# Optimization experiments

Measured on AMD Instinct MI355X. Metric: run time of the kernel, lower is better.

Reference implementation:

```python
import jax, jax.numpy as jnp
import numpy as np

HEAD_SIZE = 64


def setup_inputs() -> dict:
    key = jax.random.key(0)
    kx, kq, kk, kv = jax.random.split(key, 4)
    B, L, D = 4, 4096, 1024
    scale = 1.0 / np.sqrt(D)
    x = jax.random.normal(kx, (B, L, D), dtype=jnp.float32)
    Wq = jax.random.normal(kq, (D, HEAD_SIZE), dtype=jnp.float32) * scale
    Wk = jax.random.normal(kk, (D, HEAD_SIZE), dtype=jnp.float32) * scale
    Wv = jax.random.normal(kv, (D, HEAD_SIZE), dtype=jnp.float32) * scale
    return {"x": x, "Wq": Wq, "Wk": Wk, "Wv": Wv}


def reference(x, Wq, Wk, Wv):
    B, L, D = x.shape
    H = Wq.shape[1]
    q = jnp.einsum('bld,dh->blh', x, Wq)  # [B,L,H]
    k = jnp.einsum('bld,dh->blh', x, Wk)
    v = jnp.einsum('bld,dh->blh', x, Wv)
    # full L x L score matrix, as in the original module
    scores = jnp.einsum('bqh,bkh->bqk', q, k) / jnp.sqrt(jnp.float32(H))
    causal = jnp.tril(jnp.ones((L, L), dtype=bool))
    scores = jnp.where(causal, scores, -jnp.inf)
    attn = jax.nn.softmax(scores, axis=-1)
    z = jnp.einsum('bqk,bkh->bqh', attn, v)  # [B,L,H]
    return z
```

## Files before the change

kernel.cpp:

```cpp
#include <hip/hip_runtime.h>
#include <stdint.h>

#define L_SEQ 4096
#define D_MODEL 1024
#define HEAD 64
#define KCH 256
#define MAXCH 16
#define NQT 32

typedef unsigned short u16;
typedef _Float16 f16;
typedef __attribute__((ext_vector_type(8))) f16 f16x8;
typedef __attribute__((ext_vector_type(2))) __fp16 fp16x2;
typedef __attribute__((ext_vector_type(4))) float f32x4;

static __device__ __forceinline__ u16 f16bits(float f) {
    union { f16 h; u16 u; } c; c.h = (f16)f; return c.u;
}
static __device__ __forceinline__ uint32_t pk16(float a, float b) {
    union { fp16x2 h; uint32_t u; } c;
    c.h = __builtin_amdgcn_cvt_pkrtz(a, b);
    return c.u;
}
static __device__ __forceinline__ f16x8 ld8h(const u16* p) { return *(const f16x8*)p; }

static __device__ __forceinline__ f32x4 mfma16h(f16x8 a, f16x8 b, f32x4 c) {
    return __builtin_amdgcn_mfma_f32_16x16x32_f16(a, b, c, 0, 0, 0);
}

static __device__ __forceinline__ void gload16(const u16* g, u16* l) {
    __builtin_amdgcn_global_load_lds(
        (const __attribute__((address_space(1))) void*)g,
        (__attribute__((address_space(3))) void*)l, 16, 0, 0);
}

static __device__ __forceinline__ int Sq(int qt) {
    return (qt & 1) ? ((qt + 1) * (qt + 1)) >> 2 : (qt * (qt + 2)) >> 2;
}

__global__ __launch_bounds__(256) void conv_w(
    const float* __restrict__ Wq, const float* __restrict__ Wk,
    const float* __restrict__ Wv, u16* __restrict__ Wt)
{
    __shared__ u16 tile[64][72];
    const float* W = (blockIdx.y == 0) ? Wq : (blockIdx.y == 1) ? Wk : Wv;
    const float sc = (blockIdx.y == 0) ? 0.18033688f : 1.0f;
    u16* dst = Wt + blockIdx.y * (HEAD * D_MODEL);
    const int k0 = blockIdx.x * 64, t = threadIdx.x;
    #pragma unroll
    for (int i = 0; i < 16; i++) {
        int idx = i * 256 + t;
        int kk = idx >> 6, h = idx & 63;
        tile[h][kk] = f16bits(W[(size_t)(k0 + kk) * HEAD + h] * sc);
    }
    __syncthreads();
    #pragma unroll
    for (int i = 0; i < 16; i++) {
        int idx = i * 256 + t;
        int h = idx >> 6, kk = idx & 63;
        dst[(size_t)h * D_MODEL + k0 + kk] = tile[h][kk];
    }
}

__global__ __launch_bounds__(256) void qkv_proj(
    const float* __restrict__ x, const u16* __restrict__ Wt,
    u16* __restrict__ qb, u16* __restrict__ kb, u16* __restrict__ vTb)
{
    __shared__ __align__(16) u16 Wl[2 * 2 * 192 * 32];
    __shared__ __align__(16) u16 Xl[2 * 2 * 32 * 36];
#define WLX(bb,dh,r,c) Wl[(((bb)*2 + (dh))*192 + (r))*32 + (c)]
#define XLX(bb,kh,r,c) Xl[(((bb)*2 + (kh))*32  + (r))*36 + (c)]
#define CT(r,c)        ((u16*)Wl)[(r)*200 + (c)]

    const int t = threadIdx.x;
    const int wv = t >> 6, lane = t & 63;
    const int ln16 = lane & 15, quad = lane >> 4;
    const int w3 = wv * 3;
    const int m0 = blockIdx.x * 32;

    f32x4 acc[2][3] = {};
    float4 xv0, xv1;

    auto issueW = [&](int s, int bb) {
        const int k0 = s * 64;
        #pragma unroll
        for (int k2 = 0; k2 < 6; k2++) {
            int c = wv * 6 + k2;
            int dh = c & 1, g = c >> 1;
            const u16* gp = Wt + (size_t)(g * 16 + (lane >> 2)) * D_MODEL
                               + k0 + dh * 32 + (lane & 3) * 8;
            gload16(gp, &WLX(bb, dh, g * 16 + (lane >> 2), (lane & 3) * 8));
        }
    };
    auto loadx = [&](int s) {
        const int k0 = s * 64;
        int r0 = t >> 4, cs0 = (t & 15) * 4;
        xv0 = *(const float4*)&x[(size_t)(m0 + r0) * D_MODEL + k0 + cs0];
        int idx = 256 + t, r1 = idx >> 4, cs1 = (idx & 15) * 4;
        xv1 = *(const float4*)&x[(size_t)(m0 + r1) * D_MODEL + k0 + cs1];
    };
    auto packx = [&](int bb) {
        int r0 = t >> 4, cs0 = (t & 15) * 4;
        uint2 p0; p0.x = pk16(xv0.x, xv0.y); p0.y = pk16(xv0.z, xv0.w);
        *(uint2*)&XLX(bb, cs0 >> 5, r0, cs0 & 31) = p0;
        int idx = 256 + t, r1 = idx >> 4, cs1 = (idx & 15) * 4;
        uint2 p1; p1.x = pk16(xv1.x, xv1.y); p1.y = pk16(xv1.z, xv1.w);
        *(uint2*)&XLX(bb, cs1 >> 5, r1, cs1 & 31) = p1;
    };

    loadx(0); issueW(0, 0); packx(0);
    int buf = 0;
    for (int s = 0; s < 16; s++) {
        __syncthreads();
        f16x8 xb[2][2], af[2][3];
        #pragma unroll
        for (int c = 0; c < 2; c++) {
            xb[c][0] = ld8h(&XLX(buf, c, ln16, quad * 8));
            xb[c][1] = ld8h(&XLX(buf, c, 16 + ln16, quad * 8));
            #pragma unroll
            for (int j = 0; j < 3; j++)
                af[c][j] = ld8h(&WLX(buf, c, (w3 + j) * 16 + ln16, quad * 8));
        }
        if (s + 1 < 16) { loadx(s + 1); issueW(s + 1, buf ^ 1); }
        #pragma unroll
        for (int c = 0; c < 2; c++)
            #pragma unroll
            for (int j = 0; j < 3; j++) {
                acc[0][j] = mfma16h(af[c][j], xb[c][0], acc[0][j]);
                acc[1][j] = mfma16h(af[c][j], xb[c][1], acc[1][j]);
            }
        if (s + 1 < 16) packx(buf ^ 1);
        buf ^= 1;
    }

    __syncthreads();
    #pragma unroll
    for (int mt = 0; mt < 2; mt++) {
        #pragma unroll
        for (int j = 0; j < 3; j++) {
            int g0 = (w3 + j) * 16 + quad * 4;
            uint2 pk;
            pk.x = pk16(acc[mt][j][0], acc[mt][j][1]);
            pk.y = pk16(acc[mt][j][2], acc[mt][j][3]);
            *(uint2*)&CT(mt * 16 + ln16, g0) = pk;
        }
    }
    __syncthreads();
    {
        int m = t >> 3, hg = (t & 7) * 8;
        *(f16x8*)&qb[(size_t)(m0 + m) * HEAD + hg] = *(f16x8*)&CT(m, hg);
        *(f16x8*)&kb[(size_t)(m0 + m) * HEAD + hg] = *(f16x8*)&CT(m, 64 + hg);
        int h = t >> 2, mg = (t & 3) * 8;
        f16x8 vvv;
        #pragma unroll
        for (int jj = 0; jj < 8; jj++)
            ((u16*)&vvv)[jj] = CT(mg + jj, 128 + h);
        int bbt = m0 >> 12, l0 = m0 & 4095;
        *(f16x8*)&vTb[(size_t)(bbt * HEAD + h) * L_SEQ + l0 + mg] = vvv;
    }
#undef WLX
#undef XLX
#undef CT
}

__global__ __launch_bounds__(256, 4) void attn_chunk(
    const u16* __restrict__ qb, const u16* __restrict__ kb,
    const u16* __restrict__ vT, float* __restrict__ Opart, float* __restrict__ lpart)
{
    const int qt = blockIdx.x, ch = blockIdx.y, b = blockIdx.z;
    if (ch * KCH > qt * 128 + 127) return;

    __shared__ __align__(16) u16 Kls[2 * 64 * 32];
    __shared__ __align__(16) u16 Vls[2 * 64 * 32];
    __shared__ __align__(16) u16 Pls[4 * 32 * 72];
#define KBX(dh,r,c) Kls[((dh)*64 + (r))*32 + (c)]
#define VBX(kh,r,c) Vls[((kh)*64 + (r))*32 + (c)]
#define PX(r,c)     Pls[((wv)*32 + (r))*72 + (c)]

    const int t = threadIdx.x, wv = t >> 6, lane = t & 63;
    const int ln16 = lane & 15, quad = lane >> 4;
    const int qmin = qt * 128 + wv * 32;

    f16x8 qf[2][2];
    #pragma unroll
    for (int qn = 0; qn < 2; qn++) {
        const u16* qrp = qb + (size_t)(b * L_SEQ + qmin + qn * 16 + ln16) * HEAD + quad * 8;
        qf[qn][0] = ld8h(qrp); qf[qn][1] = ld8h(qrp + 32);
    }

    const u16* kbb = kb + (size_t)b * L_SEQ * HEAD;
    const u16* vbb = vT + (size_t)b * HEAD * L_SEQ;

    f32x4 o[2][4] = {};
    float lsum[2] = {0.f, 0.f};

    const int kv_lo = ch * KCH;
    const int kv_hi = min(kv_lo + KCH, qt * 128 + 128);
    const int nst = (kv_hi - kv_lo) >> 6;

    auto issue_stage = [&](int kv0) {
        #pragma unroll
        for (int k2 = 0; k2 < 4; k2++) {
            int c = wv * 4 + k2;
            if (c < 8) {
                int dh = c & 1, g = c >> 1;
                const u16* gp = kbb + (size_t)(kv0 + g * 16 + (lane >> 2)) * HEAD
                                    + dh * 32 + (lane & 3) * 8;
                gload16(gp, &KBX(dh, g * 16 + (lane >> 2), (lane & 3) * 8));
            } else {
                int c2 = c - 8, kh = c2 & 1, g = c2 >> 1;
                const u16* gp = vbb + (size_t)(g * 16 + (lane >> 2)) * L_SEQ
                                    + kv0 + kh * 32 + (lane & 3) * 8;
                gload16(gp, &VBX(kh, g * 16 + (lane >> 2), (lane & 3) * 8));
            }
        }
    };

    for (int s = 0; s < nst; s++) {
        const int kv0 = kv_lo + s * 64;
        issue_stage(kv0);
        __syncthreads();

        #pragma unroll
        for (int g = 0; g < 4; g++) {
            f16x8 ka0 = ld8h(&KBX(0, g * 16 + ln16, quad * 8));
            f16x8 ka1 = ld8h(&KBX(1, g * 16 + ln16, quad * 8));
            #pragma unroll
            for (int qn = 0; qn < 2; qn++) {
                f32x4 s2 = {};
                s2 = mfma16h(ka0, qf[qn][0], s2);
                s2 = mfma16h(ka1, qf[qn][1], s2);
                float p0, p1, p2, p3;
                if (kv0 + g * 16 + 15 <= qmin + qn * 16) {
                    p0 = __builtin_amdgcn_exp2f(s2[0]);
                    p1 = __builtin_amdgcn_exp2f(s2[1]);
                    p2 = __builtin_amdgcn_exp2f(s2[2]);
                    p3 = __builtin_amdgcn_exp2f(s2[3]);
                } else {
                    int q = qmin + qn * 16 + ln16;
                    int kv = kv0 + g * 16 + quad * 4;
                    p0 = (kv     <= q) ? __builtin_amdgcn_exp2f(s2[0]) : 0.f;
                    p1 = (kv + 1 <= q) ? __builtin_amdgcn_exp2f(s2[1]) : 0.f;
                    p2 = (kv + 2 <= q) ? __builtin_amdgcn_exp2f(s2[2]) : 0.f;
                    p3 = (kv + 3 <= q) ? __builtin_amdgcn_exp2f(s2[3]) : 0.f;
                }
                lsum[qn] += (p0 + p1) + (p2 + p3);
                uint2 pk; pk.x = pk16(p0, p1); pk.y = pk16(p2, p3);
                *(uint2*)&PX(qn * 16 + ln16, g * 16 + quad * 4) = pk;
            }
        }
        f16x8 pf[2][2];
        #pragma unroll
        for (int qn = 0; qn < 2; qn++) {
            pf[qn][0] = ld8h(&PX(qn * 16 + ln16, quad * 8));
            pf[qn][1] = ld8h(&PX(qn * 16 + ln16, 32 + quad * 8));
        }
        #pragma unroll
        for (int hg = 0; hg < 4; hg++) {
            f16x8 va0 = ld8h(&VBX(0, hg * 16 + ln16, quad * 8));
            f16x8 va1 = ld8h(&VBX(1, hg * 16 + ln16, quad * 8));
            #pragma unroll
            for (int qn = 0; qn < 2; qn++) {
                o[qn][hg] = mfma16h(va0, pf[qn][0], o[qn][hg]);
                o[qn][hg] = mfma16h(va1, pf[qn][1], o[qn][hg]);
            }
        }
        __syncthreads();
    }

    #pragma unroll
    for (int qn = 0; qn < 2; qn++) {
        lsum[qn] += __shfl_xor(lsum[qn], 16);
        lsum[qn] += __shfl_xor(lsum[qn], 32);
    }

    const size_t base = (size_t)(b * 272 + Sq(qt) + ch);
    #pragma unroll
    for (int qn = 0; qn < 2; qn++) {
        int q_local = wv * 32 + qn * 16 + ln16;
        #pragma unroll
        for (int hg = 0; hg < 4; hg++)
            *(f32x4*)&Opart[base * 8192 + (size_t)q_local * 64 + hg * 16 + quad * 4] = o[qn][hg];
        if (quad == 0)
            lpart[base * 128 + q_local] = lsum[qn];
    }
#undef KBX
#undef VBX
#undef PX
}

__global__ __launch_bounds__(256) void merge_chunks(
    const float* __restrict__ Opart, const float* __restrict__ lpart,
    float* __restrict__ out)
{
    const int qt = blockIdx.x, qseg = blockIdx.y, b = blockIdx.z;
    const int nch = (qt + 2) >> 1;
    const int t = threadIdx.x;
    const size_t obase = (size_t)(b * 272 + Sq(qt)) * 8192;
    const size_t lbase = (size_t)(b * 272 + Sq(qt)) * 128;
    #pragma unroll
    for (int i = 0; i < 2; i++) {
        int idx = i * 256 + t;
        int q = qseg * 32 + (idx >> 4), hg = (idx & 15) * 4;
        float L = 0.f, ax = 0.f, ay = 0.f, az = 0.f, aw = 0.f;
        #pragma unroll
        for (int c = 0; c < MAXCH; c++) {
            if (c < nch) {
                L += lpart[lbase + c * 128 + q];
                const float4 v = *(const float4*)&Opart[obase + (size_t)c * 8192 + q * 64 + hg];
                ax += v.x; ay += v.y; az += v.z; aw += v.w;
            }
        }
        float inv = 1.f / L;
        float4 r; r.x = ax * inv; r.y = ay * inv; r.z = az * inv; r.w = aw * inv;
        *(float4*)&out[((size_t)(b * L_SEQ + qt * 128 + q)) * HEAD + hg] = r;
    }
}

extern "C" void kernel_launch(void* const* d_in, const int* in_sizes, int n_in,
                              void* d_out, int out_size, void* d_ws, size_t ws_size,
                              hipStream_t stream) {
    const float* x  = (const float*)d_in[0];
    const float* Wq = (const float*)d_in[1];
    const float* Wk = (const float*)d_in[2];
    const float* Wv = (const float*)d_in[3];
    float* out = (float*)d_out;

    u16* ws16 = (u16*)d_ws;
    u16* Wt  = ws16;
    u16* qb  = Wt + 3 * HEAD * D_MODEL;
    u16* kb  = qb + 16384 * HEAD;
    u16* vTb = kb + 16384 * HEAD;
    float* Opart = (float*)(vTb + 16384 * HEAD);
    float* lpart = Opart + (size_t)4 * 272 * 8192;

    conv_w      <<<dim3(16, 3), 256, 0, stream>>>(Wq, Wk, Wv, Wt);
    qkv_proj    <<<dim3(512), 256, 0, stream>>>(x, Wt, qb, kb, vTb);
    attn_chunk  <<<dim3(NQT, MAXCH, 4), 256, 0, stream>>>(qb, kb, vTb, Opart, lpart);
    merge_chunks<<<dim3(NQT, 4, 4), 256, 0, stream>>>(Opart, lpart, out);
}
```

Measured before the change: 167.1 us.

## Double KV chunk size to halve partial outputs; single-buffer projection LDS

Doubles the attention key/value chunk length from 256 to 512, so each query tile is split into half as many partial chunks. This shrinks the Opart/lpart partial buffers and the merge work, and Sq/base indexing is updated to match. The QKV projection kernel is also changed from double-buffered to single-buffered LDS with an extra barrier and a 4-block occupancy hint, trading load/compute overlap for more resident blocks. Fewer chunks means less grid parallelism in attention and longer per-block work.

```diff
diff --git a/kernel.cpp b/kernel.cpp
--- a/kernel.cpp
+++ b/kernel.cpp
@@ -4,8 +4,8 @@
 #define L_SEQ 4096
 #define D_MODEL 1024
 #define HEAD 64
-#define KCH 256
-#define MAXCH 16
+#define KCH 512
+#define MAXCH 8
 #define NQT 32
 
 typedef unsigned short u16;
@@ -35,7 +35,8 @@
 }
 
 static __device__ __forceinline__ int Sq(int qt) {
-    return (qt & 1) ? ((qt + 1) * (qt + 1)) >> 2 : (qt * (qt + 2)) >> 2;
+    int f = qt >> 2, r = qt & 3;
+    return (f + 1) * (2 * f + r);
 }
 
 __global__ __launch_bounds__(256) void conv_w(
@@ -62,15 +63,15 @@
     }
 }
 
-__global__ __launch_bounds__(256) void qkv_proj(
+__global__ __launch_bounds__(256, 4) void qkv_proj(
     const float* __restrict__ x, const u16* __restrict__ Wt,
     u16* __restrict__ qb, u16* __restrict__ kb, u16* __restrict__ vTb)
 {
-    __shared__ __align__(16) u16 Wl[2 * 2 * 192 * 32];
-    __shared__ __align__(16) u16 Xl[2 * 2 * 32 * 36];
-#define WLX(bb,dh,r,c) Wl[(((bb)*2 + (dh))*192 + (r))*32 + (c)]
-#define XLX(bb,kh,r,c) Xl[(((bb)*2 + (kh))*32  + (r))*36 + (c)]
-#define CT(r,c)        ((u16*)Wl)[(r)*200 + (c)]
+    __shared__ __align__(16) u16 Wl[2 * 192 * 32];
+    __shared__ __align__(16) u16 Xl[2 * 32 * 36];
+#define WLX(dh,r,c) Wl[((dh)*192 + (r))*32 + (c)]
+#define XLX(kh,r,c) Xl[((kh)*32  + (r))*36 + (c)]
+#define CT(r,c)     Wl[(r)*200 + (c)]
 
     const int t = threadIdx.x;
     const int wv = t >> 6, lane = t & 63;
@@ -81,7 +82,7 @@
     f32x4 acc[2][3] = {};
     float4 xv0, xv1;
 
-    auto issueW = [&](int s, int bb) {
+    auto issueW = [&](int s) {
         const int k0 = s * 64;
         #pragma unroll
         for (int k2 = 0; k2 < 6; k2++) {
@@ -89,7 +90,7 @@
             int dh = c & 1, g = c >> 1;
             const u16* gp = Wt + (size_t)(g * 16 + (lane >> 2)) * D_MODEL
                                + k0 + dh * 32 + (lane & 3) * 8;
-            gload16(gp, &WLX(bb, dh, g * 16 + (lane >> 2), (lane & 3) * 8));
+            gload16(gp, &WLX(dh, g * 16 + (lane >> 2), (lane & 3) * 8));
         }
     };
     auto loadx = [&](int s) {
@@ -99,29 +100,27 @@
         int idx = 256 + t, r1 = idx >> 4, cs1 = (idx & 15) * 4;
         xv1 = *(const float4*)&x[(size_t)(m0 + r1) * D_MODEL + k0 + cs1];
     };
-    auto packx = [&](int bb) {
+    auto packx = [&]() {
         int r0 = t >> 4, cs0 = (t & 15) * 4;
         uint2 p0; p0.x = pk16(xv0.x, xv0.y); p0.y = pk16(xv0.z, xv0.w);
-        *(uint2*)&XLX(bb, cs0 >> 5, r0, cs0 & 31) = p0;
+        *(uint2*)&XLX(cs0 >> 5, r0, cs0 & 31) = p0;
         int idx = 256 + t, r1 = idx >> 4, cs1 = (idx & 15) * 4;
         uint2 p1; p1.x = pk16(xv1.x, xv1.y); p1.y = pk16(xv1.z, xv1.w);
-        *(uint2*)&XLX(bb, cs1 >> 5, r1, cs1 & 31) = p1;
+        *(uint2*)&XLX(cs1 >> 5, r1, cs1 & 31) = p1;
     };
 
-    loadx(0); issueW(0, 0); packx(0);
-    int buf = 0;
+    loadx(0); issueW(0); packx();
     for (int s = 0; s < 16; s++) {
         __syncthreads();
         f16x8 xb[2][2], af[2][3];
         #pragma unroll
         for (int c = 0; c < 2; c++) {
-            xb[c][0] = ld8h(&XLX(buf, c, ln16, quad * 8));
-            xb[c][1] = ld8h(&XLX(buf, c, 16 + ln16, quad * 8));
+            xb[c][0] = ld8h(&XLX(c, ln16, quad * 8));
+            xb[c][1] = ld8h(&XLX(c, 16 + ln16, quad * 8));
             #pragma unroll
             for (int j = 0; j < 3; j++)
-                af[c][j] = ld8h(&WLX(buf, c, (w3 + j) * 16 + ln16, quad * 8));
-        }
-        if (s + 1 < 16) { loadx(s + 1); issueW(s + 1, buf ^ 1); }
+                af[c][j] = ld8h(&WLX(c, (w3 + j) * 16 + ln16, quad * 8));
+        }
         #pragma unroll
         for (int c = 0; c < 2; c++)
             #pragma unroll
@@ -129,8 +128,9 @@
                 acc[0][j] = mfma16h(af[c][j], xb[c][0], acc[0][j]);
                 acc[1][j] = mfma16h(af[c][j], xb[c][1], acc[1][j]);
             }
-        if (s + 1 < 16) packx(buf ^ 1);
-        buf ^= 1;
+        if (s + 1 < 16) loadx(s + 1);
+        __syncthreads();
+        if (s + 1 < 16) { issueW(s + 1); packx(); }
     }
 
     __syncthreads();
@@ -274,7 +274,7 @@
         lsum[qn] += __shfl_xor(lsum[qn], 32);
     }
 
-    const size_t base = (size_t)(b * 272 + Sq(qt) + ch);
+    const size_t base = (size_t)(b * 144 + Sq(qt) + ch);
     #pragma unroll
     for (int qn = 0; qn < 2; qn++) {
         int q_local = wv * 32 + qn * 16 + ln16;
@@ -294,10 +294,10 @@
     float* __restrict__ out)
 {
     const int qt = blockIdx.x, qseg = blockIdx.y, b = blockIdx.z;
-    const int nch = (qt + 2) >> 1;
+    const int nch = (qt + 4) >> 2;
     const int t = threadIdx.x;
-    const size_t obase = (size_t)(b * 272 + Sq(qt)) * 8192;
-    const size_t lbase = (size_t)(b * 272 + Sq(qt)) * 128;
+    const size_t obase = (size_t)(b * 144 + Sq(qt)) * 8192;
+    const size_t lbase = (size_t)(b * 144 + Sq(qt)) * 128;
     #pragma unroll
     for (int i = 0; i < 2; i++) {
         int idx = i * 256 + t;
@@ -332,7 +332,7 @@
     u16* kb  = qb + 16384 * HEAD;
     u16* vTb = kb + 16384 * HEAD;
     float* Opart = (float*)(vTb + 16384 * HEAD);
-    float* lpart = Opart + (size_t)4 * 272 * 8192;
+    float* lpart = Opart + (size_t)4 * 144 * 8192;
 
     conv_w      <<<dim3(16, 3), 256, 0, stream>>>(Wq, Wk, Wv, Wt);
     qkv_proj    <<<dim3(512), 256, 0, stream>>>(x, Wt, qb, kb, vTb);
```

Measured after the change: 152.7 us. 8.6% less time.
